# Optimization experiments

Hardware: AMD Instinct MI355X
Metric: run time of the kernel (lower is better)

Reference implementation:

```python
import jax, jax.numpy as jnp
import numpy as np

N_NODES = 40000
N_EDGES = 640000
D = 128


def setup_inputs() -> dict:
    key = jax.random.key(0)
    ks = jax.random.split(key, 7)
    x = jax.random.normal(ks[0], (N_NODES, D), dtype=jnp.float32)
    edge_index = jax.random.randint(ks[1], (2, N_EDGES), 0, N_NODES, dtype=jnp.int64)
    # uniform in [0.5, 1.5) to avoid division blow-up near zero
    edge_attr = jax.random.uniform(ks[2], (N_EDGES,), dtype=jnp.float32) + 0.5
    s = 1.0 / np.sqrt(D)
    W1 = jax.random.uniform(ks[3], (D, D), dtype=jnp.float32, minval=-s, maxval=s)
    b1 = jax.random.uniform(ks[4], (D,), dtype=jnp.float32, minval=-s, maxval=s)
    W2 = jax.random.uniform(ks[5], (D, D), dtype=jnp.float32, minval=-s, maxval=s)
    b2 = jax.random.uniform(ks[6], (D,), dtype=jnp.float32, minval=-s, maxval=s)
    return {"x": x, "edge_index": edge_index, "edge_attr": edge_attr,
            "W1": W1, "b1": b1, "W2": W2, "b2": b2}


def _layer(x, src, dst, edge_attr, W, b, num_nodes):
    # message: gather source features, divide by per-edge scalar
    msg = x[src] / edge_attr[:, None]                      # [E, D]
    # aggregate: scatter-add into destination nodes
    agg = jax.ops.segment_sum(msg, dst, num_segments=num_nodes)  # [N, D]
    # linear (torch: y = x @ W.T + b) then leaky_relu(0.01)
    y = agg @ W.T + b
    return jnp.where(y >= 0, y, 0.01 * y)


def reference(x, edge_index, edge_attr, W1, b1, W2, b2):
    src, dst = edge_index[0], edge_index[1]
    n = x.shape[0]
    x = jnp.maximum(_layer(x, src, dst, edge_attr, W1, b1, n), 0.0)
    x = jnp.maximum(_layer(x, src, dst, edge_attr, W2, b2, n), 0.0)
    return x
```

## Files before the change

### kernel.cpp

```cpp
#include <hip/hip_runtime.h>

#define D 128
#define CAP 64
typedef unsigned short u16;
typedef unsigned int   u32;

typedef __attribute__((ext_vector_type(8))) short short8;
typedef __attribute__((ext_vector_type(4))) float f32x4;

__device__ __forceinline__ u32 f2bf(float f) {
    u32 u = __float_as_uint(f);
    u += 0x7fffu + ((u >> 16) & 1u);
    return u >> 16;
}
__device__ __forceinline__ float2 bf2x2(u32 u) {
    float2 r;
    r.x = __uint_as_float(u << 16);
    r.y = __uint_as_float(u & 0xffff0000u);
    return r;
}

__global__ __launch_bounds__(256) void prep_kernel(
    const float4* __restrict__ x, uint2* __restrict__ xb,
    const float4* __restrict__ W1, const float4* __restrict__ W2,
    uint2* __restrict__ wb1, uint2* __restrict__ wb2,
    const int* __restrict__ src, const int* __restrict__ dst,
    const float* __restrict__ attr, int* __restrict__ counts,
    u32* __restrict__ combo, int E, int n4, int cvtb)
{
    const int bid = blockIdx.x;
    const int t   = threadIdx.x;

    if (bid < cvtb) {
        int i = bid * 256 + t;
        if (i < n4) {
            float4 v = x[i];
            uint2 o;
            o.x = f2bf(v.x) | (f2bf(v.y) << 16);
            o.y = f2bf(v.z) | (f2bf(v.w) << 16);
            xb[i] = o;
        }
    } else if (bid < cvtb + 32) {
        int i = (bid - cvtb) * 256 + t;
        const float4* in = (i < 4096) ? W1 : W2;
        uint2* out = (i < 4096) ? wb1 : wb2;
        int k = i & 4095;
        float4 v = in[k];
        uint2 o;
        o.x = f2bf(v.x) | (f2bf(v.y) << 16);
        o.y = f2bf(v.z) | (f2bf(v.w) << 16);
        out[k] = o;
    } else {
        int e0 = (bid - cvtb - 32) * 1024 + t;
        int   d[4]; float iv[4]; int s[4]; int r[4]; bool ok[4];
        #pragma unroll
        for (int q = 0; q < 4; ++q) {
            int e = e0 + q * 256;
            ok[q] = e < E;
            if (ok[q]) { d[q] = dst[e]; s[q] = src[e]; iv[q] = attr[e]; }
        }
        #pragma unroll
        for (int q = 0; q < 4; ++q)
            if (ok[q]) r[q] = atomicAdd(&counts[d[q]], 1);
        #pragma unroll
        for (int q = 0; q < 4; ++q)
            if (ok[q] && r[q] < CAP) {
                u32 v = (u32)s[q] | (f2bf(1.0f / iv[q]) << 16);
                combo[((long long)d[q] << 6) + r[q]] = v;
            }
    }
}

__global__ __launch_bounds__(256) void gather_kernel(
    const u16* __restrict__ x, const u32* __restrict__ combo,
    const int* __restrict__ counts, u16* __restrict__ agg, int N)
{
    const int node = (blockIdx.x * 256 + threadIdx.x) >> 6;
    if (node >= N) return;
    const int lane = threadIdx.x & 63;

    const int cnt = min(counts[node], CAP);
    const u32 ce = combo[((long long)node << 6) + lane];

    float a0 = 0.f, a1 = 0.f, b0 = 0.f, b1 = 0.f;
    float c0 = 0.f, c1 = 0.f, d0 = 0.f, d1 = 0.f;

    int j = 0;
    for (; j + 3 < cnt; j += 4) {
        u32 eA = __shfl(ce, j + 0);
        u32 eB = __shfl(ce, j + 1);
        u32 eC = __shfl(ce, j + 2);
        u32 eD = __shfl(ce, j + 3);
        u32 r0 = *(const u32*)(x + (long long)(eA & 0xffffu) * D + lane * 2);
        u32 r1 = *(const u32*)(x + (long long)(eB & 0xffffu) * D + lane * 2);
        u32 r2 = *(const u32*)(x + (long long)(eC & 0xffffu) * D + lane * 2);
        u32 r3 = *(const u32*)(x + (long long)(eD & 0xffffu) * D + lane * 2);
        float f0 = __uint_as_float(eA & 0xffff0000u);
        float f1 = __uint_as_float(eB & 0xffff0000u);
        float f2 = __uint_as_float(eC & 0xffff0000u);
        float f3 = __uint_as_float(eD & 0xffff0000u);
        float2 v0 = bf2x2(r0), v1 = bf2x2(r1), v2 = bf2x2(r2), v3 = bf2x2(r3);
        a0 += v0.x * f0; a1 += v0.y * f0;
        b0 += v1.x * f1; b1 += v1.y * f1;
        c0 += v2.x * f2; c1 += v2.y * f2;
        d0 += v3.x * f3; d1 += v3.y * f3;
    }
    for (; j < cnt; ++j) {
        u32 eA = __shfl(ce, j);
        u32 r0 = *(const u32*)(x + (long long)(eA & 0xffffu) * D + lane * 2);
        float f0 = __uint_as_float(eA & 0xffff0000u);
        float2 v0 = bf2x2(r0);
        a0 += v0.x * f0; a1 += v0.y * f0;
    }

    float s0 = (a0 + b0) + (c0 + d0);
    float s1 = (a1 + b1) + (c1 + d1);
    u32 o = f2bf(s0) | (f2bf(s1) << 16);
    *(u32*)(agg + (long long)node * D + lane * 2) = o;
}

template <bool OUT_BF16>
__global__ __launch_bounds__(256) void mfma_gemm_kernel(
    const u16* __restrict__ A, const u16* __restrict__ Wb,
    const float* __restrict__ b, void* __restrict__ Yv, int N)
{
    const int wv   = threadIdx.x >> 6;
    const int lane = threadIdx.x & 63;
    const int m0   = (blockIdx.x * 4 + wv) * 16;
    const int mrow = lane & 15;
    const int kq   = lane >> 4;

    const u16* arow = A + (long long)(m0 + mrow) * D + kq * 8;
    short8 afr[4];
    #pragma unroll
    for (int ks = 0; ks < 4; ++ks)
        afr[ks] = *(const short8*)(arow + ks * 32);

    #pragma unroll 1
    for (int j = 0; j < 8; ++j) {
        float bias = b[j * 16 + mrow];
        f32x4 acc = {bias, bias, bias, bias};
        const u16* wrow = Wb + (long long)(j * 16 + mrow) * D + kq * 8;
        #pragma unroll
        for (int ks = 0; ks < 4; ++ks) {
            short8 bfr = *(const short8*)(wrow + ks * 32);
            acc = __builtin_amdgcn_mfma_f32_16x16x32_bf16(afr[ks], bfr, acc, 0, 0, 0);
        }
        #pragma unroll
        for (int r = 0; r < 4; ++r) {
            float v = acc[r] > 0.f ? acc[r] : 0.f;
            int row = m0 + kq * 4 + r;
            int col = j * 16 + mrow;
            if (OUT_BF16)
                *((u16*)Yv + (long long)row * D + col) = (u16)f2bf(v);
            else
                *((float*)Yv + (long long)row * D + col) = v;
        }
    }
}

extern "C" void kernel_launch(void* const* d_in, const int* in_sizes, int n_in,
                              void* d_out, int out_size, void* d_ws, size_t ws_size,
                              hipStream_t stream)
{
    const float* x    = (const float*)d_in[0];
    const int*   eidx = (const int*)d_in[1];
    const float* attr = (const float*)d_in[2];
    const float* W1   = (const float*)d_in[3];
    const float* b1   = (const float*)d_in[4];
    const float* W2   = (const float*)d_in[5];
    const float* b2   = (const float*)d_in[6];

    const int N = in_sizes[0] / D;
    const int E = in_sizes[2];
    const int* src = eidx;
    const int* dst = eidx + E;

    char* p = (char*)d_ws;
    u16*  xb    = (u16*)p;   p += ((size_t)N * D * 2 + 15) & ~15ULL;
    u16*  aggB  = (u16*)p;   p += ((size_t)N * D * 2 + 15) & ~15ULL;
    u32*  combo = (u32*)p;   p += (size_t)N * CAP * 4;
    u16*  wb1   = (u16*)p;   p += (size_t)D * D * 2;
    u16*  wb2   = (u16*)p;   p += (size_t)D * D * 2;
    int*  counts= (int*)p;

    const int n4    = N * D / 4;
    const int cvtb  = (n4 + 255) / 256;
    const int hfb   = (E + 1023) / 1024;
    const int prepb = cvtb + 32 + hfb;
    const int gatherb = (N + 3) / 4;
    const int gemmb   = N / 64;

    hipMemsetAsync(counts, 0, (size_t)N * 4, stream);
    prep_kernel<<<prepb, 256, 0, stream>>>(
        (const float4*)x, (uint2*)xb, (const float4*)W1, (const float4*)W2,
        (uint2*)wb1, (uint2*)wb2, src, dst, attr, counts,
        combo, E, n4, cvtb);

    gather_kernel<<<gatherb, 256, 0, stream>>>(xb, combo, counts, aggB, N);
    mfma_gemm_kernel<true><<<gemmb, 256, 0, stream>>>(aggB, wb1, b1, aggB, N);

    gather_kernel<<<gatherb, 256, 0, stream>>>(aggB, combo, counts, xb, N);
    mfma_gemm_kernel<false><<<gemmb, 256, 0, stream>>>(xb, wb2, b2, d_out, N);
}
```

Before: 204.8 us.

## Fuse neighbor gather-aggregate into MFMA GEMM per layer

Merges the gather/segment-sum kernel and the bf16 MFMA linear kernel into one kernel per layer. Each lane set accumulates the aggregated row directly into the MFMA A-fragment layout (16 nodes per wave, 4 lanes per node reading 16-byte chunks). This removes the intermediate aggregate write/read and two launches. In exchange, the gather now has only 16 nodes per wave with a serial per-edge loop bounded by the wave's max degree, so divergence and lower memory-level parallelism may make the gather slower.

Measured after the change: 215.4 us. 5.2% more time.

```diff
diff --git a/kernel.cpp b/kernel.cpp
--- a/kernel.cpp
+++ b/kernel.cpp
@@ -71,90 +71,87 @@
     }
 }
 
-__global__ __launch_bounds__(256) void gather_kernel(
-    const u16* __restrict__ x, const u32* __restrict__ combo,
-    const int* __restrict__ counts, u16* __restrict__ agg, int N)
-{
-    const int node = (blockIdx.x * 256 + threadIdx.x) >> 6;
-    if (node >= N) return;
-    const int lane = threadIdx.x & 63;
-
-    const int cnt = min(counts[node], CAP);
-    const u32 ce = combo[((long long)node << 6) + lane];
-
-    float a0 = 0.f, a1 = 0.f, b0 = 0.f, b1 = 0.f;
-    float c0 = 0.f, c1 = 0.f, d0 = 0.f, d1 = 0.f;
-
-    int j = 0;
-    for (; j + 3 < cnt; j += 4) {
-        u32 eA = __shfl(ce, j + 0);
-        u32 eB = __shfl(ce, j + 1);
-        u32 eC = __shfl(ce, j + 2);
-        u32 eD = __shfl(ce, j + 3);
-        u32 r0 = *(const u32*)(x + (long long)(eA & 0xffffu) * D + lane * 2);
-        u32 r1 = *(const u32*)(x + (long long)(eB & 0xffffu) * D + lane * 2);
-        u32 r2 = *(const u32*)(x + (long long)(eC & 0xffffu) * D + lane * 2);
-        u32 r3 = *(const u32*)(x + (long long)(eD & 0xffffu) * D + lane * 2);
-        float f0 = __uint_as_float(eA & 0xffff0000u);
-        float f1 = __uint_as_float(eB & 0xffff0000u);
-        float f2 = __uint_as_float(eC & 0xffff0000u);
-        float f3 = __uint_as_float(eD & 0xffff0000u);
-        float2 v0 = bf2x2(r0), v1 = bf2x2(r1), v2 = bf2x2(r2), v3 = bf2x2(r3);
-        a0 += v0.x * f0; a1 += v0.y * f0;
-        b0 += v1.x * f1; b1 += v1.y * f1;
-        c0 += v2.x * f2; c1 += v2.y * f2;
-        d0 += v3.x * f3; d1 += v3.y * f3;
-    }
-    for (; j < cnt; ++j) {
-        u32 eA = __shfl(ce, j);
-        u32 r0 = *(const u32*)(x + (long long)(eA & 0xffffu) * D + lane * 2);
-        float f0 = __uint_as_float(eA & 0xffff0000u);
-        float2 v0 = bf2x2(r0);
-        a0 += v0.x * f0; a1 += v0.y * f0;
-    }
-
-    float s0 = (a0 + b0) + (c0 + d0);
-    float s1 = (a1 + b1) + (c1 + d1);
-    u32 o = f2bf(s0) | (f2bf(s1) << 16);
-    *(u32*)(agg + (long long)node * D + lane * 2) = o;
-}
-
 template <bool OUT_BF16>
-__global__ __launch_bounds__(256) void mfma_gemm_kernel(
-    const u16* __restrict__ A, const u16* __restrict__ Wb,
-    const float* __restrict__ b, void* __restrict__ Yv, int N)
+__global__ __launch_bounds__(256) void fused_layer_kernel(
+    const u16* __restrict__ X, const u32* __restrict__ combo,
+    const int* __restrict__ counts, const u16* __restrict__ Wb,
+    const float* __restrict__ bias, void* __restrict__ Yv, int N)
 {
     const int wv   = threadIdx.x >> 6;
     const int lane = threadIdx.x & 63;
     const int m0   = (blockIdx.x * 4 + wv) * 16;
-    const int mrow = lane & 15;
+    const int m    = lane & 15;
     const int kq   = lane >> 4;
-
-    const u16* arow = A + (long long)(m0 + mrow) * D + kq * 8;
+    const int node = m0 + m;
+
+    const int cnt = (node < N) ? min(counts[node], CAP) : 0;
+
+    int cmax = cnt;
+    cmax = max(cmax, __shfl_xor(cmax, 1));
+    cmax = max(cmax, __shfl_xor(cmax, 2));
+    cmax = max(cmax, __shfl_xor(cmax, 4));
+    cmax = max(cmax, __shfl_xor(cmax, 8));
+
+    float acc[4][8];
+    #pragma unroll
+    for (int ks = 0; ks < 4; ++ks)
+        #pragma unroll
+        for (int i = 0; i < 8; ++i) acc[ks][i] = 0.f;
+
+    const long long cbase = (long long)node << 6;
+    u32 e = (cnt > 0) ? combo[cbase] : 0u;
+
+    for (int j = 0; j < cmax; ++j) {
+        u32 cur = e;
+        if (j + 1 < cnt) e = combo[cbase + j + 1];
+        if (j < cnt) {
+            const u16* row = X + (long long)(cur & 0xffffu) * D + kq * 8;
+            float f = __uint_as_float(cur & 0xffff0000u);
+            #pragma unroll
+            for (int ks = 0; ks < 4; ++ks) {
+                uint4 r = *(const uint4*)(row + ks * 32);
+                float2 v0 = bf2x2(r.x), v1 = bf2x2(r.y);
+                float2 v2 = bf2x2(r.z), v3 = bf2x2(r.w);
+                acc[ks][0] += v0.x * f; acc[ks][1] += v0.y * f;
+                acc[ks][2] += v1.x * f; acc[ks][3] += v1.y * f;
+                acc[ks][4] += v2.x * f; acc[ks][5] += v2.y * f;
+                acc[ks][6] += v3.x * f; acc[ks][7] += v3.y * f;
+            }
+        }
+    }
+
     short8 afr[4];
     #pragma unroll
-    for (int ks = 0; ks < 4; ++ks)
-        afr[ks] = *(const short8*)(arow + ks * 32);
+    for (int ks = 0; ks < 4; ++ks) {
+        u32 p0 = f2bf(acc[ks][0]) | (f2bf(acc[ks][1]) << 16);
+        u32 p1 = f2bf(acc[ks][2]) | (f2bf(acc[ks][3]) << 16);
+        u32 p2 = f2bf(acc[ks][4]) | (f2bf(acc[ks][5]) << 16);
+        u32 p3 = f2bf(acc[ks][6]) | (f2bf(acc[ks][7]) << 16);
+        uint4 packed = {p0, p1, p2, p3};
+        afr[ks] = *(short8*)&packed;
+    }
 
     #pragma unroll 1
-    for (int j = 0; j < 8; ++j) {
-        float bias = b[j * 16 + mrow];
-        f32x4 acc = {bias, bias, bias, bias};
-        const u16* wrow = Wb + (long long)(j * 16 + mrow) * D + kq * 8;
+    for (int jj = 0; jj < 8; ++jj) {
+        float bv = bias[jj * 16 + m];
+        f32x4 c = {bv, bv, bv, bv};
+        const u16* wrow = Wb + (long long)(jj * 16 + m) * D + kq * 8;
         #pragma unroll
         for (int ks = 0; ks < 4; ++ks) {
             short8 bfr = *(const short8*)(wrow + ks * 32);
-            acc = __builtin_amdgcn_mfma_f32_16x16x32_bf16(afr[ks], bfr, acc, 0, 0, 0);
+            c = __builtin_amdgcn_mfma_f32_16x16x32_bf16(afr[ks], bfr, c, 0, 0, 0);
         }
         #pragma unroll
         for (int r = 0; r < 4; ++r) {
-            float v = acc[r] > 0.f ? acc[r] : 0.f;
+            float v = c[r] > 0.f ? c[r] : 0.f;
             int row = m0 + kq * 4 + r;
-            int col = j * 16 + mrow;
-            if (OUT_BF16)
-                *((u16*)Yv + (long long)row * D + col) = (u16)f2bf(v);
-            else
-                *((float*)Yv + (long long)row * D + col) = v;
+            int col = jj * 16 + m;
+            if (row < N) {
+                if (OUT_BF16)
+                    *((u16*)Yv + (long long)row * D + col) = (u16)f2bf(v);
+                else
+                    *((float*)Yv + (long long)row * D + col) = v;
+            }
         }
     }
 }
@@ -188,8 +185,7 @@
     const int cvtb  = (n4 + 255) / 256;
     const int hfb   = (E + 1023) / 1024;
     const int prepb = cvtb + 32 + hfb;
-    const int gatherb = (N + 3) / 4;
-    const int gemmb   = N / 64;
+    const int fblocks = (N + 63) / 64;
 
     hipMemsetAsync(counts, 0, (size_t)N * 4, stream);
     prep_kernel<<<prepb, 256, 0, stream>>>(
@@ -197,9 +193,8 @@
         (uint2*)wb1, (uint2*)wb2, src, dst, attr, counts,
         combo, E, n4, cvtb);
 
-    gather_kernel<<<gatherb, 256, 0, stream>>>(xb, combo, counts, aggB, N);
-    mfma_gemm_kernel<true><<<gemmb, 256, 0, stream>>>(aggB, wb1, b1, aggB, N);
-
-    gather_kernel<<<gatherb, 256, 0, stream>>>(aggB, combo, counts, xb, N);
-    mfma_gemm_kernel<false><<<gemmb, 256, 0, stream>>>(xb, wb2, b2, d_out, N);
-}
+    fused_layer_kernel<true><<<fblocks, 256, 0, stream>>>(
+        xb, combo, counts, wb1, b1, aggB, N);
+    fused_layer_kernel<false><<<fblocks, 256, 0, stream>>>(
+        aggB, combo, counts, wb2, b2, d_out, N);
+}
```
